# Performance work log

Measured on AMD Instinct MI355X. Metric: run time of the kernel, lower is better.

## Reference

```python
import jax, jax.numpy as jnp
import numpy as np

C = 256
HEADS = 8
HEAD_DIM = C // HEADS
GROUPS = 8
EPS = 1e-5


def setup_inputs() -> dict:
    key = jax.random.key(0)
    ks = jax.random.split(key, 11)
    B, S = 2, 16
    s = 0.02
    return {
        "x": jax.random.normal(ks[0], (B, C, S, S, S), dtype=jnp.float32),
        "gn_w": jnp.ones((C,), jnp.float32),
        "gn_b": jnp.zeros((C,), jnp.float32),
        "wq": jax.random.normal(ks[1], (C, C), jnp.float32) * s,
        "bq": jnp.zeros((C,), jnp.float32),
        "wk": jax.random.normal(ks[2], (C, C), jnp.float32) * s,
        "bk": jnp.zeros((C,), jnp.float32),
        "wv": jax.random.normal(ks[3], (C, C), jnp.float32) * s,
        "bv": jnp.zeros((C,), jnp.float32),
        "wo": jax.random.normal(ks[4], (C, C), jnp.float32) * s,
        "bo": jnp.zeros((C,), jnp.float32),
    }


def _group_norm(x, w, b):
    # x: [B, C, D, H, W]; GroupNorm(8, C) with affine params
    B, Cc, D, H, W = x.shape
    xg = x.reshape(B, GROUPS, Cc // GROUPS, D, H, W)
    mu = jnp.mean(xg, axis=(2, 3, 4, 5), keepdims=True)
    var = jnp.mean(jnp.square(xg - mu), axis=(2, 3, 4, 5), keepdims=True)
    xn = ((xg - mu) * jax.lax.rsqrt(var + EPS)).reshape(B, Cc, D, H, W)
    return xn * w[None, :, None, None, None] + b[None, :, None, None, None]


def reference(x, gn_w, gn_b, wq, bq, wk, bk, wv, bv, wo, bo):
    B, Cc, D, H, W = x.shape
    N = D * H * W
    xn = _group_norm(x, gn_w, gn_b).reshape(B, Cc, N)  # [B,C,N]
    # 1x1x1 Conv3d == per-voxel linear: weight [out,in]
    Q = jnp.einsum("oc,bcn->bon", wq, xn) + bq[None, :, None]
    K = jnp.einsum("oc,bcn->bon", wk, xn) + bk[None, :, None]
    V = jnp.einsum("oc,bcn->bon", wv, xn) + bv[None, :, None]
    Q = Q.reshape(B, HEADS, HEAD_DIM, N)
    K = K.reshape(B, HEADS, HEAD_DIM, N)
    V = V.reshape(B, HEADS, HEAD_DIM, N)
    scale = np.sqrt(HEAD_DIM).astype(np.float32)
    attn = jnp.einsum("bhdn,bhdm->bhnm", Q, K) / scale
    attn = jax.nn.softmax(attn, axis=-1)
    out = jnp.einsum("bhnm,bhdm->bhdn", attn, V)  # [B,h,hd,N]
    out = out.reshape(B, Cc, N)
    out = jnp.einsum("oc,bcn->bon", wo, out) + bo[None, :, None]
    return x + out.reshape(B, Cc, D, H, W)
```

## Files before the change

kernel.cpp:

```cpp
#include <hip/hip_runtime.h>

#define B_   2
#define C_   256
#define N_   4096
#define H_   8
#define HD_  32
#define G_   8
#define CPG_ 32

typedef short short8 __attribute__((ext_vector_type(8)));
typedef float f32x4  __attribute__((ext_vector_type(4)));
typedef float f4     __attribute__((ext_vector_type(4)));

__device__ __forceinline__ float b2f(short s) {
    return __uint_as_float(((unsigned)(unsigned short)s) << 16);
}
__device__ __forceinline__ short f2b(float f) {
    unsigned u = __float_as_uint(f);
    unsigned r = (u + 0x7FFF + ((u >> 16) & 1)) >> 16;
    return (short)r;
}

__global__ __launch_bounds__(256) void gn_part(const float* __restrict__ x,
                                               float* __restrict__ part) {
    int blk = blockIdx.x;
    const f4* p = (const f4*)x + (size_t)(blk >> 6) * (CPG_ * N_ / 4) + (size_t)(blk & 63) * 512;
    float s = 0.f, ss = 0.f;
#pragma unroll
    for (int i = 0; i < 2; i++) {
        f4 v = p[threadIdx.x + i * 256];
#pragma unroll
        for (int j = 0; j < 4; j++) { float f = v[j]; s += f; ss += f * f; }
    }
#pragma unroll
    for (int off = 32; off > 0; off >>= 1) {
        s  += __shfl_down(s, off);
        ss += __shfl_down(ss, off);
    }
    __shared__ float rs[4], rss[4];
    int w = threadIdx.x >> 6;
    if ((threadIdx.x & 63) == 0) { rs[w] = s; rss[w] = ss; }
    __syncthreads();
    if (threadIdx.x == 0) {
        part[blk * 2]     = rs[0] + rs[1] + rs[2] + rs[3];
        part[blk * 2 + 1] = rss[0] + rss[1] + rss[2] + rss[3];
    }
}

__global__ __launch_bounds__(256) void gemm_qkv(
    const float* __restrict__ x,
    const float* __restrict__ gw, const float* __restrict__ gb,
    const float* __restrict__ part,
    const float* __restrict__ wq, const float* __restrict__ bq,
    const float* __restrict__ wk, const float* __restrict__ bk,
    const float* __restrict__ wv, const float* __restrict__ bv,
    short* __restrict__ q, short* __restrict__ kt, short* __restrict__ v) {
    int z = blockIdx.z;
    int b = z / 3, which = z % 3;
    const float* W    = which == 0 ? wq : (which == 1 ? wk : wv);
    const float* bias = which == 0 ? bq : (which == 1 ? bk : bv);
    bool trans = (which != 2);
    float mul = (which == 0) ? (0.17677669529663687f * 1.4426950408889634f) : 1.0f;

    __shared__ short wl[64][40];
    __shared__ short xl[128][40];
    __shared__ float ga[256], gbb[256];
    __shared__ float mus[8], rstds[8];

    int o0 = blockIdx.y * 64, n0 = blockIdx.x * 128;
    int tid = threadIdx.x;
    int w = tid >> 6, lane = tid & 63, li = lane & 15, quad = lane >> 4;
    int wr = w & 1, wc = w >> 1;

#pragma unroll
    for (int gi = 0; gi < 2; gi++) {
        int g = w * 2 + gi;
        const float* pp = &part[(size_t)(b * 8 + g) * 128 + lane * 2];
        float s = pp[0], ss = pp[1];
#pragma unroll
        for (int off = 32; off > 0; off >>= 1) {
            s  += __shfl_down(s, off);
            ss += __shfl_down(ss, off);
        }
        if (lane == 0) {
            const float inv = 1.f / (float)(CPG_ * N_);
            float mu = s * inv;
            float var = ss * inv - mu * mu;
            mus[g] = mu;
            rstds[g] = rsqrtf(var + 1e-5f);
        }
    }
    __syncthreads();
    {
        int c = tid, g = c >> 5;
        float a = rstds[g] * gw[c];
        ga[c]  = a;
        gbb[c] = gb[c] - mus[g] * a;
    }

    f32x4 acc[8];
#pragma unroll
    for (int i = 0; i < 8; i++) acc[i] = (f32x4){0.f, 0.f, 0.f, 0.f};

    int cpair = tid >> 4, l16 = tid & 15;
    __syncthreads();

    for (int k0 = 0; k0 < 256; k0 += 32) {
        {
            int row = tid >> 2, co = (tid & 3) << 3;
            const float* wp = &W[(size_t)(o0 + row) * 256 + k0 + co];
            f4 wa = *(const f4*)wp;
            f4 wb = *(const f4*)(wp + 4);
            short8 w8;
#pragma unroll
            for (int j = 0; j < 4; j++) { w8[j] = f2b(wa[j]); w8[j + 4] = f2b(wb[j]); }
            *(short8*)&wl[row][co] = w8;
        }
        {
            int c0 = k0 + cpair * 2;
            float a0 = ga[c0],     b0c = gbb[c0];
            float a1 = ga[c0 + 1], b1c = gbb[c0 + 1];
            const float* xr0 = x + ((size_t)(b * 256 + c0)) * N_ + n0 + l16;
            const float* xr1 = xr0 + N_;
#pragma unroll
            for (int j = 0; j < 8; j++) {
                unsigned lo = (unsigned short)f2b(xr0[16 * j] * a0 + b0c);
                unsigned hi = (unsigned short)f2b(xr1[16 * j] * a1 + b1c);
                *(unsigned*)&xl[l16 + 16 * j][cpair * 2] = lo | (hi << 16);
            }
        }
        __syncthreads();
        short8 af[4], bfr[4];
        if (trans) {
#pragma unroll
            for (int i = 0; i < 4; i++) af[i]  = *(short8*)&xl[wr * 64 + i * 16 + li][quad * 8];
#pragma unroll
            for (int j = 0; j < 2; j++) bfr[j] = *(short8*)&wl[wc * 32 + j * 16 + li][quad * 8];
#pragma unroll
            for (int i = 0; i < 4; i++)
#pragma unroll
                for (int j = 0; j < 2; j++)
                    acc[i * 2 + j] = __builtin_amdgcn_mfma_f32_16x16x32_bf16(af[i], bfr[j], acc[i * 2 + j], 0, 0, 0);
        } else {
#pragma unroll
            for (int i = 0; i < 2; i++) af[i]  = *(short8*)&wl[wr * 32 + i * 16 + li][quad * 8];
#pragma unroll
            for (int j = 0; j < 4; j++) bfr[j] = *(short8*)&xl[wc * 64 + j * 16 + li][quad * 8];
#pragma unroll
            for (int i = 0; i < 2; i++)
#pragma unroll
                for (int j = 0; j < 4; j++)
                    acc[i * 4 + j] = __builtin_amdgcn_mfma_f32_16x16x32_bf16(af[i], bfr[j], acc[i * 4 + j], 0, 0, 0);
        }
        __syncthreads();
    }

    if (which == 2) {
        short* outp = v + (size_t)b * C_ * N_;
#pragma unroll
        for (int i = 0; i < 2; i++) {
            int ob = o0 + wr * 32 + i * 16 + quad * 4;
#pragma unroll
            for (int j = 0; j < 4; j++) {
                int n_ = n0 + wc * 64 + j * 16 + li;
#pragma unroll
                for (int r = 0; r < 4; r++) {
                    float val = acc[i * 4 + j][r] + bias[ob + r];
                    outp[(size_t)(ob + r) * N_ + n_] = f2b(val);
                }
            }
        }
    } else if (which == 0) {
        short* outp = q + (size_t)b * N_ * C_;
#pragma unroll
        for (int i = 0; i < 4; i++) {
            int nb_ = n0 + wr * 64 + i * 16 + quad * 4;
#pragma unroll
            for (int j = 0; j < 2; j++) {
                int o_ = o0 + wc * 32 + j * 16 + li;
                float bv_ = bias[o_];
#pragma unroll
                for (int r = 0; r < 4; r++)
                    outp[(size_t)(nb_ + r) * C_ + o_] = f2b((acc[i * 2 + j][r] + bv_) * mul);
            }
        }
    } else {
#pragma unroll
        for (int i = 0; i < 4; i++) {
            int nb_ = n0 + wr * 64 + i * 16 + quad * 4;
#pragma unroll
            for (int j = 0; j < 2; j++) {
                int o_ = o0 + wc * 32 + j * 16 + li;
                int hh = o_ >> 5, d = o_ & 31;
                float bv_ = bias[o_];
                short* kdst = kt + ((size_t)(b * 8 + hh) * N_) * HD_ + d;
#pragma unroll
                for (int r = 0; r < 4; r++)
                    kdst[(size_t)(nb_ + r) * HD_] = f2b(acc[i * 2 + j][r] + bv_);
            }
        }
    }
}

#define STAGE_BARRIER(bufk, bufv)                                         \
    *(short8*)&kl[(bufk) * 2560 + klo] = kst;                             \
    *(short8*)&vl[(bufv) * 2304 + vlo] = vst;                             \
    __syncthreads();

#define PREFETCH(t1)                                                      \
    kst = *(const short8*)(kgp + (size_t)(t1) * 64 * HD_);                \
    vst = *(const short8*)(vgp + (t1) * 64);

#define LOADVF(vf, bufv)                                                  \
    vf[0] = *(short8*)&vl[(bufv) * 2304 + li * 72 + quad * 8];            \
    vf[1] = *(short8*)&vl[(bufv) * 2304 + (16 + li) * 72 + quad * 8];     \
    vf[2] = *(short8*)&vl[(bufv) * 2304 + li * 72 + 32 + quad * 8];       \
    vf[3] = *(short8*)&vl[(bufv) * 2304 + (16 + li) * 72 + 32 + quad * 8];

#define QK(bufk)                                                          \
    _Pragma("unroll")                                                     \
    for (int c = 0; c < 4; c++) {                                         \
        short8 kf = *(short8*)&kl[(bufk) * 2560 + (c * 16 + li) * 40 + quad * 8]; \
        s0[c] = __builtin_amdgcn_mfma_f32_16x16x32_bf16(kf, qf0, zero, 0, 0, 0);  \
        s1[c] = __builtin_amdgcn_mfma_f32_16x16x32_bf16(kf, qf1, zero, 0, 0, 0);  \
    }

#define PV(pP, vf)                                                        \
    {                                                                     \
        short8 pf00 = *(short8*)&(pP)[li * 72 + quad * 8];                \
        short8 pf01 = *(short8*)&(pP)[li * 72 + 32 + quad * 8];           \
        short8 pf10 = *(short8*)&(pP)[1152 + li * 72 + quad * 8];         \
        short8 pf11 = *(short8*)&(pP)[1152 + li * 72 + 32 + quad * 8];    \
        oa00 = __builtin_amdgcn_mfma_f32_16x16x32_bf16(pf00, vf[0], oa00, 0, 0, 0); \
        oa01 = __builtin_amdgcn_mfma_f32_16x16x32_bf16(pf00, vf[1], oa01, 0, 0, 0); \
        oa00 = __builtin_amdgcn_mfma_f32_16x16x32_bf16(pf01, vf[2], oa00, 0, 0, 0); \
        oa01 = __builtin_amdgcn_mfma_f32_16x16x32_bf16(pf01, vf[3], oa01, 0, 0, 0); \
        oa10 = __builtin_amdgcn_mfma_f32_16x16x32_bf16(pf10, vf[0], oa10, 0, 0, 0); \
        oa11 = __builtin_amdgcn_mfma_f32_16x16x32_bf16(pf10, vf[1], oa11, 0, 0, 0); \
        oa10 = __builtin_amdgcn_mfma_f32_16x16x32_bf16(pf11, vf[2], oa10, 0, 0, 0); \
        oa11 = __builtin_amdgcn_mfma_f32_16x16x32_bf16(pf11, vf[3], oa11, 0, 0, 0); \
    }

#define EXPPACK(pC)                                                       \
    {                                                                     \
        float lp = 0.f;                                                   \
        _Pragma("unroll")                                                 \
        for (int c = 0; c < 4; c++) {                                     \
            float e0 = __builtin_amdgcn_exp2f(s0[c][0]);                  \
            float e1 = __builtin_amdgcn_exp2f(s0[c][1]);                  \
            float e2 = __builtin_amdgcn_exp2f(s0[c][2]);                  \
            float e3 = __builtin_amdgcn_exp2f(s0[c][3]);                  \
            lp += (e0 + e1) + (e2 + e3);                                  \
            unsigned pk0 = __builtin_amdgcn_perm(__float_as_uint(e1), __float_as_uint(e0), 0x07060302); \
            unsigned pk1 = __builtin_amdgcn_perm(__float_as_uint(e3), __float_as_uint(e2), 0x07060302); \
            uint2 pkv; pkv.x = pk0; pkv.y = pk1;                          \
            *(uint2*)&(pC)[li * 72 + c * 16 + quad * 4] = pkv;            \
        }                                                                 \
        lr0 += lp;                                                        \
        lp = 0.f;                                                         \
        _Pragma("unroll")                                                 \
        for (int c = 0; c < 4; c++) {                                     \
            float e0 = __builtin_amdgcn_exp2f(s1[c][0]);                  \
            float e1 = __builtin_amdgcn_exp2f(s1[c][1]);                  \
            float e2 = __builtin_amdgcn_exp2f(s1[c][2]);                  \
            float e3 = __builtin_amdgcn_exp2f(s1[c][3]);                  \
            lp += (e0 + e1) + (e2 + e3);                                  \
            unsigned pk0 = __builtin_amdgcn_perm(__float_as_uint(e1), __float_as_uint(e0), 0x07060302); \
            unsigned pk1 = __builtin_amdgcn_perm(__float_as_uint(e3), __float_as_uint(e2), 0x07060302); \
            uint2 pkv; pkv.x = pk0; pkv.y = pk1;                          \
            *(uint2*)&(pC)[1152 + li * 72 + c * 16 + quad * 4] = pkv;     \
        }                                                                 \
        lr1 += lp;                                                        \
    }

__global__ __launch_bounds__(256) void flash(const short* __restrict__ q,
                                             const short* __restrict__ ktp,
                                             const short* __restrict__ v,
                                             short* __restrict__ aoT) {
    int bid = blockIdx.x;
    int xcd = bid & 7;
    int s_  = bid >> 3;
    int bh  = xcd * 2 + (s_ & 1);
    int nb  = s_ >> 1;
    int b = bh >> 3, h = bh & 7;

    const short* QT = q   + (size_t)b * N_ * C_ + h * HD_;
    const short* KP = ktp + (size_t)bh * N_ * HD_;
    const short* V  = v   + ((size_t)b * C_ + h * HD_) * N_;
    short* O = aoT + (size_t)b * N_ * C_ + h * HD_;

    __shared__ short kl[2 * 2560];
    __shared__ short vl[2 * 2304];
    __shared__ short pl[4 * 4608];

    int tid = threadIdx.x, w = tid >> 6, lane = tid & 63, li = lane & 15, quad = lane >> 4;
    int n0w = nb * 128 + w * 32;
    short* pA = pl + w * 4608;
    short* pB = pA + 2304;

    short8 qf0 = *(const short8*)&QT[(size_t)(n0w + li) * 256 + quad * 8];
    short8 qf1 = *(const short8*)&QT[(size_t)(n0w + 16 + li) * 256 + quad * 8];

    f32x4 oa00 = (f32x4){0.f,0.f,0.f,0.f}, oa01 = oa00, oa10 = oa00, oa11 = oa00;
    float lr0 = 0.f, lr1 = 0.f;
    const f32x4 zero = (f32x4){0.f, 0.f, 0.f, 0.f};

    int krow = tid >> 2, kcol = (tid & 3) << 3;
    int vrow = tid >> 3, vcol = (tid & 7) << 3;
    const short* kgp = KP + (size_t)krow * HD_ + kcol;
    const short* vgp = V + (size_t)vrow * N_ + vcol;
    int klo = krow * 40 + kcol;
    int vlo = vrow * 72 + vcol;

    short8 kst = *(const short8*)kgp;
    short8 vst = *(const short8*)vgp;
    short8 vfa[4], vfb[4];
    f32x4 s0[4], s1[4];

    STAGE_BARRIER(0, 0);
    PREFETCH(1);
    LOADVF(vfa, 0);
    QK(0);
    EXPPACK(pA);

    for (int mt = 1; mt < 62; mt += 2) {
        STAGE_BARRIER(1, 1);
        PREFETCH(mt + 1);
        LOADVF(vfb, 1);
        QK(1);
        PV(pA, vfa);
        EXPPACK(pB);
        STAGE_BARRIER(0, 0);
        PREFETCH(mt + 2);
        LOADVF(vfa, 0);
        QK(0);
        PV(pB, vfb);
        EXPPACK(pA);
    }
    STAGE_BARRIER(1, 1);
    LOADVF(vfb, 1);
    QK(1);
    PV(pA, vfa);
    EXPPACK(pB);
    PV(pB, vfb);

    lr0 += __shfl_xor(lr0, 16); lr0 += __shfl_xor(lr0, 32);
    lr1 += __shfl_xor(lr1, 16); lr1 += __shfl_xor(lr1, 32);
#pragma unroll
    for (int r2 = 0; r2 < 4; r2++) {
        float ln0 = __shfl(lr0, quad * 4 + r2);
        float inv0 = 1.f / ln0;
        size_t n_ = (size_t)(n0w + quad * 4 + r2);
        O[n_ * 256 + li]      = f2b(oa00[r2] * inv0);
        O[n_ * 256 + 16 + li] = f2b(oa01[r2] * inv0);
        float ln1 = __shfl(lr1, quad * 4 + r2);
        float inv1 = 1.f / ln1;
        size_t n2 = (size_t)(n0w + 16 + quad * 4 + r2);
        O[n2 * 256 + li]      = f2b(oa10[r2] * inv1);
        O[n2 * 256 + 16 + li] = f2b(oa11[r2] * inv1);
    }
}

__global__ __launch_bounds__(256) void gemm_out(const float* __restrict__ W,
                                                const float* __restrict__ bias,
                                                const short* __restrict__ aoT,
                                                const float* __restrict__ resid,
                                                float* __restrict__ out) {
    int b = blockIdx.z;
    const short* X = aoT + (size_t)b * N_ * C_;
    const float* R = resid + (size_t)b * C_ * N_;
    float* outp = out + (size_t)b * C_ * N_;

    __shared__ short wl[128][40];
    __shared__ short xl[64][40];

    int o0 = blockIdx.y * 128, n0 = blockIdx.x * 64;
    int tid = threadIdx.x;
    int w = tid >> 6, lane = tid & 63, li = lane & 15, quad = lane >> 4;
    int wr = w & 1, wc = w >> 1;

    f32x4 acc[4][2];
#pragma unroll
    for (int i = 0; i < 4; i++)
#pragma unroll
        for (int j = 0; j < 2; j++) acc[i][j] = (f32x4){0.f, 0.f, 0.f, 0.f};

    for (int k0 = 0; k0 < 256; k0 += 32) {
#pragma unroll
        for (int i = 0; i < 2; i++) {
            int idx = tid + i * 256;
            int row = idx >> 2, co = (idx & 3) << 3;
            const float* wp = &W[(size_t)(o0 + row) * 256 + k0 + co];
            f4 wa = *(const f4*)wp;
            f4 wb = *(const f4*)(wp + 4);
            short8 w8;
#pragma unroll
            for (int j = 0; j < 4; j++) { w8[j] = f2b(wa[j]); w8[j + 4] = f2b(wb[j]); }
            *(short8*)&wl[row][co] = w8;
        }
        {
            int row = tid >> 2, co = (tid & 3) << 3;
            *(short8*)&xl[row][co] = *(const short8*)&X[(size_t)(n0 + row) * 256 + k0 + co];
        }
        __syncthreads();
        short8 af[4], bfr[2];
#pragma unroll
        for (int i = 0; i < 4; i++) af[i]  = *(short8*)&wl[wr * 64 + i * 16 + li][quad * 8];
#pragma unroll
        for (int j = 0; j < 2; j++) bfr[j] = *(short8*)&xl[wc * 32 + j * 16 + li][quad * 8];
#pragma unroll
        for (int i = 0; i < 4; i++)
#pragma unroll
            for (int j = 0; j < 2; j++)
                acc[i][j] = __builtin_amdgcn_mfma_f32_16x16x32_bf16(af[i], bfr[j], acc[i][j], 0, 0, 0);
        __syncthreads();
    }
#pragma unroll
    for (int i = 0; i < 4; i++) {
        int ob = o0 + wr * 64 + i * 16 + quad * 4;
#pragma unroll
        for (int j = 0; j < 2; j++) {
            int n_ = n0 + wc * 32 + j * 16 + li;
#pragma unroll
            for (int r = 0; r < 4; r++) {
                size_t idx = (size_t)(ob + r) * N_ + n_;
                outp[idx] = acc[i][j][r] + bias[ob + r] + R[idx];
            }
        }
    }
}

extern "C" void kernel_launch(void* const* d_in, const int* in_sizes, int n_in,
                              void* d_out, int out_size, void* d_ws, size_t ws_size,
                              hipStream_t stream) {
    const float* x  = (const float*)d_in[0];
    const float* gw = (const float*)d_in[1];
    const float* gb = (const float*)d_in[2];
    const float* wq = (const float*)d_in[3];
    const float* bq = (const float*)d_in[4];
    const float* wk = (const float*)d_in[5];
    const float* bk = (const float*)d_in[6];
    const float* wv = (const float*)d_in[7];
    const float* bv = (const float*)d_in[8];
    const float* wo = (const float*)d_in[9];
    const float* bo = (const float*)d_in[10];
    float* out = (float*)d_out;

    char* ws = (char*)d_ws;
    float* part = (float*)ws;
    const size_t TS = (size_t)B_ * N_ * C_;
    short* aoT = (short*)(ws + 16384);
    short* q   = aoT + TS;
    short* kt  = q + TS;
    short* v   = kt + TS;

    gn_part<<<1024, 256, 0, stream>>>(x, part);
    gemm_qkv<<<dim3(32, 4, 6), 256, 0, stream>>>(x, gw, gb, part,
                                                 wq, bq, wk, bk, wv, bv, q, kt, v);
    flash<<<512, 256, 0, stream>>>(q, kt, v, aoT);
    gemm_out<<<dim3(64, 2, 2), 256, 0, stream>>>(wo, bo, aoT, x, out);
}
```

Before: 172.1 us.

## Halve flash-attention block size to two waves and single-buffer the P tile

Flash-attention blocks now have 128 threads (two waves, 64 query rows) instead of 256 threads (four waves, 128 rows), and the grid doubles to 1024 blocks. Each thread now stages two K and two V chunks per tile. The per-wave P tile becomes single-buffered: each step runs QK, then PV on the previous P, then writes the new P, reordered so the LDS reads come before the overwrite. This cuts LDS use per block and gives a finer-grained grid, but each block re-reads the full K and V for half as many queries, which doubles K/V global and L2 traffic.

```diff
diff --git a/kernel.cpp b/kernel.cpp
--- a/kernel.cpp
+++ b/kernel.cpp
@@ -202,14 +202,21 @@
     }
 }
 
-#define STAGE_BARRIER(bufk, bufv)                                         \
-    *(short8*)&kl[(bufk) * 2560 + klo] = kst;                             \
-    *(short8*)&vl[(bufv) * 2304 + vlo] = vst;                             \
+#define STAGE_BARRIER(buf)                                                \
+    *(short8*)&kl[(buf) * 2560 + klo] = kst0;                             \
+    *(short8*)&kl[(buf) * 2560 + klo + 32 * 40] = kst1;                   \
+    *(short8*)&vl[(buf) * 2304 + vlo] = vst0;                             \
+    *(short8*)&vl[(buf) * 2304 + vlo + 16 * 72] = vst1;                   \
     __syncthreads();
 
 #define PREFETCH(t1)                                                      \
-    kst = *(const short8*)(kgp + (size_t)(t1) * 64 * HD_);                \
-    vst = *(const short8*)(vgp + (t1) * 64);
+    {                                                                     \
+        int m1_ = (t1) * 64;                                              \
+        kst0 = *(const short8*)(kgp + (size_t)m1_ * HD_);                 \
+        kst1 = *(const short8*)(kgp + (size_t)(m1_ + 32) * HD_);          \
+        vst0 = *(const short8*)(vgp + m1_);                               \
+        vst1 = *(const short8*)(vgp + (size_t)16 * N_ + m1_);             \
+    }
 
 #define LOADVF(vf, bufv)                                                  \
     vf[0] = *(short8*)&vl[(bufv) * 2304 + li * 72 + quad * 8];            \
@@ -225,12 +232,12 @@
         s1[c] = __builtin_amdgcn_mfma_f32_16x16x32_bf16(kf, qf1, zero, 0, 0, 0);  \
     }
 
-#define PV(pP, vf)                                                        \
+#define PV(vf)                                                            \
     {                                                                     \
-        short8 pf00 = *(short8*)&(pP)[li * 72 + quad * 8];                \
-        short8 pf01 = *(short8*)&(pP)[li * 72 + 32 + quad * 8];           \
-        short8 pf10 = *(short8*)&(pP)[1152 + li * 72 + quad * 8];         \
-        short8 pf11 = *(short8*)&(pP)[1152 + li * 72 + 32 + quad * 8];    \
+        short8 pf00 = *(short8*)&pA[li * 72 + quad * 8];                  \
+        short8 pf01 = *(short8*)&pA[li * 72 + 32 + quad * 8];             \
+        short8 pf10 = *(short8*)&pA[1152 + li * 72 + quad * 8];           \
+        short8 pf11 = *(short8*)&pA[1152 + li * 72 + 32 + quad * 8];      \
         oa00 = __builtin_amdgcn_mfma_f32_16x16x32_bf16(pf00, vf[0], oa00, 0, 0, 0); \
         oa01 = __builtin_amdgcn_mfma_f32_16x16x32_bf16(pf00, vf[1], oa01, 0, 0, 0); \
         oa00 = __builtin_amdgcn_mfma_f32_16x16x32_bf16(pf01, vf[2], oa00, 0, 0, 0); \
@@ -241,7 +248,7 @@
         oa11 = __builtin_amdgcn_mfma_f32_16x16x32_bf16(pf11, vf[3], oa11, 0, 0, 0); \
     }
 
-#define EXPPACK(pC)                                                       \
+#define EXPPACK()                                                         \
     {                                                                     \
         float lp = 0.f;                                                   \
         _Pragma("unroll")                                                 \
@@ -254,7 +261,7 @@
             unsigned pk0 = __builtin_amdgcn_perm(__float_as_uint(e1), __float_as_uint(e0), 0x07060302); \
             unsigned pk1 = __builtin_amdgcn_perm(__float_as_uint(e3), __float_as_uint(e2), 0x07060302); \
             uint2 pkv; pkv.x = pk0; pkv.y = pk1;                          \
-            *(uint2*)&(pC)[li * 72 + c * 16 + quad * 4] = pkv;            \
+            *(uint2*)&pA[li * 72 + c * 16 + quad * 4] = pkv;              \
         }                                                                 \
         lr0 += lp;                                                        \
         lp = 0.f;                                                         \
@@ -268,12 +275,12 @@
             unsigned pk0 = __builtin_amdgcn_perm(__float_as_uint(e1), __float_as_uint(e0), 0x07060302); \
             unsigned pk1 = __builtin_amdgcn_perm(__float_as_uint(e3), __float_as_uint(e2), 0x07060302); \
             uint2 pkv; pkv.x = pk0; pkv.y = pk1;                          \
-            *(uint2*)&(pC)[1152 + li * 72 + c * 16 + quad * 4] = pkv;     \
+            *(uint2*)&pA[1152 + li * 72 + c * 16 + quad * 4] = pkv;       \
         }                                                                 \
         lr1 += lp;                                                        \
     }
 
-__global__ __launch_bounds__(256) void flash(const short* __restrict__ q,
+__global__ __launch_bounds__(128) void flash(const short* __restrict__ q,
                                              const short* __restrict__ ktp,
                                              const short* __restrict__ v,
                                              short* __restrict__ aoT) {
@@ -291,12 +298,11 @@
 
     __shared__ short kl[2 * 2560];
     __shared__ short vl[2 * 2304];
-    __shared__ short pl[4 * 4608];
+    __shared__ short pl[2 * 2304];
 
     int tid = threadIdx.x, w = tid >> 6, lane = tid & 63, li = lane & 15, quad = lane >> 4;
-    int n0w = nb * 128 + w * 32;
-    short* pA = pl + w * 4608;
-    short* pB = pA + 2304;
+    int n0w = nb * 64 + w * 32;
+    short* pA = pl + w * 2304;
 
     short8 qf0 = *(const short8*)&QT[(size_t)(n0w + li) * 256 + quad * 8];
     short8 qf1 = *(const short8*)&QT[(size_t)(n0w + 16 + li) * 256 + quad * 8];
@@ -312,37 +318,39 @@
     int klo = krow * 40 + kcol;
     int vlo = vrow * 72 + vcol;
 
-    short8 kst = *(const short8*)kgp;
-    short8 vst = *(const short8*)vgp;
+    short8 kst0 = *(const short8*)kgp;
+    short8 kst1 = *(const short8*)(kgp + (size_t)32 * HD_);
+    short8 vst0 = *(const short8*)vgp;
+    short8 vst1 = *(const short8*)(vgp + (size_t)16 * N_);
     short8 vfa[4], vfb[4];
     f32x4 s0[4], s1[4];
 
-    STAGE_BARRIER(0, 0);
+    STAGE_BARRIER(0);
     PREFETCH(1);
+    QK(0);
+    EXPPACK();
     LOADVF(vfa, 0);
-    QK(0);
-    EXPPACK(pA);
 
     for (int mt = 1; mt < 62; mt += 2) {
-        STAGE_BARRIER(1, 1);
+        STAGE_BARRIER(1);
         PREFETCH(mt + 1);
+        QK(1);
+        PV(vfa);
+        EXPPACK();
         LOADVF(vfb, 1);
-        QK(1);
-        PV(pA, vfa);
-        EXPPACK(pB);
-        STAGE_BARRIER(0, 0);
+        STAGE_BARRIER(0);
         PREFETCH(mt + 2);
+        QK(0);
+        PV(vfb);
+        EXPPACK();
         LOADVF(vfa, 0);
-        QK(0);
-        PV(pB, vfb);
-        EXPPACK(pA);
-    }
-    STAGE_BARRIER(1, 1);
+    }
+    STAGE_BARRIER(1);
+    QK(1);
+    PV(vfa);
+    EXPPACK();
     LOADVF(vfb, 1);
-    QK(1);
-    PV(pA, vfa);
-    EXPPACK(pB);
-    PV(pB, vfb);
+    PV(vfb);
 
     lr0 += __shfl_xor(lr0, 16); lr0 += __shfl_xor(lr0, 32);
     lr1 += __shfl_xor(lr1, 16); lr1 += __shfl_xor(lr1, 32);
@@ -457,6 +465,6 @@
     gn_part<<<1024, 256, 0, stream>>>(x, part);
     gemm_qkv<<<dim3(32, 4, 6), 256, 0, stream>>>(x, gw, gb, part,
                                                  wq, bq, wk, bk, wv, bv, q, kt, v);
-    flash<<<512, 256, 0, stream>>>(q, kt, v, aoT);
+    flash<<<1024, 128, 0, stream>>>(q, kt, v, aoT);
     gemm_out<<<dim3(64, 2, 2), 256, 0, stream>>>(wo, bo, aoT, x, out);
 }
```

After: 175.3 us. About the same (+1.9%).
